# Performance work log

Measured on AMD Instinct MI355X. Metric: run time of the kernel, lower is better.

Reference implementation:

```python
import jax, jax.numpy as jnp
import numpy as np
import math

B, T, C = 1, 2048, 512
NH, NKV, HD, W = 8, 4, 64, 128  # heads, kv heads, head_dim, window_size
THETA = 10000.0
EPS = 1e-6


def _rms(x, w):
    # RMSNorm over last (head_dim) axis with learnable scale w
    return x * jax.lax.rsqrt(jnp.mean(x * x, axis=-1, keepdims=True) + EPS) * w


def _rope(x, cos, sin):
    # x: (B, H, T, HD); cos/sin: (T, HD//2). Half-split rotation.
    h = x.shape[-1] // 2
    x1, x2 = x[..., :h], x[..., h:]
    return jnp.concatenate([x1 * cos - x2 * sin, x2 * cos + x1 * sin], axis=-1)


def setup_inputs():
    key = jax.random.key(0)
    ks = jax.random.split(key, 5)
    x = jax.random.normal(ks[0], (B, T, C), jnp.float32)
    s = 1.0 / math.sqrt(C)
    W_q = jax.random.normal(ks[1], (C, NH * HD), jnp.float32) * s
    W_k = jax.random.normal(ks[2], (C, NKV * HD), jnp.float32) * s
    W_v = jax.random.normal(ks[3], (C, NKV * HD), jnp.float32) * s
    W_o = jax.random.normal(ks[4], (C, C), jnp.float32) * s
    q_norm_w = jnp.ones((HD,), jnp.float32)
    k_norm_w = jnp.ones((HD,), jnp.float32)
    pos = jnp.arange(T, dtype=jnp.float32)
    inv_freq = 1.0 / (THETA ** (jnp.arange(0, HD, 2, dtype=jnp.float32) / HD))
    ang = pos[:, None] * inv_freq[None, :]  # (T, HD//2)
    return {"x": x, "W_q": W_q, "W_k": W_k, "W_v": W_v, "W_o": W_o,
            "q_norm_w": q_norm_w, "k_norm_w": k_norm_w,
            "cos": jnp.cos(ang), "sin": jnp.sin(ang)}


def reference(x, W_q, W_k, W_v, W_o, q_norm_w, k_norm_w, cos, sin):
    q = (x @ W_q).reshape(B, T, NH, HD).transpose(0, 2, 1, 3)   # (B,NH,T,HD)
    k = (x @ W_k).reshape(B, T, NKV, HD).transpose(0, 2, 1, 3)  # (B,NKV,T,HD)
    v = (x @ W_v).reshape(B, T, NKV, HD).transpose(0, 2, 1, 3)
    q = _rope(q, cos, sin)
    k = _rope(k, cos, sin)
    q = _rms(q, q_norm_w)
    k = _rms(k, k_norm_w)
    g = NH // NKV  # GQA group size
    k = jnp.repeat(k, g, axis=1)  # (B,NH,T,HD)
    v = jnp.repeat(v, g, axis=1)
    # causal sliding-window: gather W-length windows ending at each position
    kp = jnp.pad(k, ((0, 0), (0, 0), (W - 1, 0), (0, 0)))
    vp = jnp.pad(v, ((0, 0), (0, 0), (W - 1, 0), (0, 0)))
    idx = jnp.arange(T)[:, None] + jnp.arange(W)[None, :]  # (T, W)
    kw = kp[:, :, idx, :]  # (B,NH,T,W,HD)
    vw = vp[:, :, idx, :]
    valid = jnp.arange(W)[None, :] >= (W - 1 - jnp.arange(T))[:, None]  # (T,W)
    attn = jnp.einsum('bhtd,bhtwd->bhtw', q, kw) / math.sqrt(HD)
    attn = jnp.where(valid[None, None], attn, -jnp.inf)
    attn = jax.nn.softmax(attn, axis=-1)
    out = jnp.einsum('bhtw,bhtwd->bhtd', attn, vw)  # (B,NH,T,HD)
    out = out.transpose(0, 2, 1, 3).reshape(B, T, C)
    return out @ W_o
```

## Files before the change

kernel.cpp:

```cpp
#include <hip/hip_runtime.h>
#include <hip/hip_bf16.h>
#include <math.h>

typedef float  f32x4  __attribute__((ext_vector_type(4)));
typedef short  s16x4  __attribute__((ext_vector_type(4)));
typedef short  s16x8  __attribute__((ext_vector_type(8)));
typedef unsigned short u16;

__device__ inline u16 f2b(float f) {
    __hip_bfloat16 h = __float2bfloat16(f);
    return *reinterpret_cast<u16*>(&h);
}
__device__ inline float b2f(u16 v) {
    return __uint_as_float(((unsigned)v) << 16);
}
__device__ inline void st_out(float* p, float v) { *p = v; }
__device__ inline void st_out(u16* p, float v)   { *p = f2b(v); }

__global__ __launch_bounds__(256) void prep(const float* __restrict__ x,
    const float* __restrict__ Wq, const float* __restrict__ Wk,
    const float* __restrict__ Wv, const float* __restrict__ Wo,
    u16* __restrict__ xb, u16* __restrict__ Wt, u16* __restrict__ Wot)
{
    const int tid = threadIdx.x, bid = blockIdx.x;
    if (bid >= 192) {
        int i = ((bid - 192) * 256 + tid) * 8;
        float4 v0 = *(const float4*)(x + i);
        float4 v1 = *(const float4*)(x + i + 4);
        ushort4 o0 = { f2b(v0.x), f2b(v0.y), f2b(v0.z), f2b(v0.w) };
        ushort4 o1 = { f2b(v1.x), f2b(v1.y), f2b(v1.z), f2b(v1.w) };
        *(ushort4*)(xb + i)     = o0;
        *(ushort4*)(xb + i + 4) = o1;
        return;
    }
    __shared__ u16 Tsh[64][72];
    const float* src; u16* dst; int N, base, kt, nt;
    if (bid < 64)       { src = Wq; dst = Wt;  N = 512; base = 0;   kt = bid >> 3;       nt = bid & 7; }
    else if (bid < 96)  { src = Wk; dst = Wt;  N = 256; base = 512; kt = (bid-64) >> 2;  nt = (bid-64) & 3; }
    else if (bid < 128) { src = Wv; dst = Wt;  N = 256; base = 768; kt = (bid-96) >> 2;  nt = (bid-96) & 3; }
    else                { src = Wo; dst = Wot; N = 512; base = 0;   kt = (bid-128) >> 3; nt = (bid-128) & 7; }
    const int k0 = kt * 64, n0 = nt * 64;
    const int r = tid >> 2, c0 = (tid & 3) * 16;
#pragma unroll
    for (int j = 0; j < 4; ++j) {
        float4 v = *(const float4*)(src + (size_t)(k0 + r) * N + n0 + c0 + j * 4);
        Tsh[c0 + j*4 + 0][r] = f2b(v.x);
        Tsh[c0 + j*4 + 1][r] = f2b(v.y);
        Tsh[c0 + j*4 + 2][r] = f2b(v.z);
        Tsh[c0 + j*4 + 3][r] = f2b(v.w);
    }
    __syncthreads();
    const int n = tid >> 2, kc = (tid & 3) * 16;
    u16* op = dst + (size_t)(base + n0 + n) * 512 + k0 + kc;
    *(s16x8*)(op)     = *(const s16x8*)&Tsh[n][kc];
    *(s16x8*)(op + 8) = *(const s16x8*)&Tsh[n][kc + 8];
}

template<typename OutT>
__global__ __launch_bounds__(256) void gemm_mfma(const u16* __restrict__ A,
    const u16* __restrict__ Bt, OutT* __restrict__ C, int ldc)
{
    __shared__ u16 Ash[64][72];
    __shared__ u16 Bsh[64][72];
    const int tid = threadIdx.x;
    const int m0b = blockIdx.y * 64, n0b = blockIdx.x * 64;
    const int lane = tid & 63, wv = tid >> 6;
    const int q = lane & 15, g = lane >> 4;
    const int wm = (wv & 1) * 32, wn = (wv >> 1) * 32;
    const int sr = tid >> 2, sc = (tid & 3) * 16;
    f32x4 acc[2][2] = {{{0,0,0,0},{0,0,0,0}},{{0,0,0,0},{0,0,0,0}}};
    for (int k0 = 0; k0 < 512; k0 += 64) {
        s16x8 a0 = *(const s16x8*)(A  + (size_t)(m0b + sr) * 512 + k0 + sc);
        s16x8 a1 = *(const s16x8*)(A  + (size_t)(m0b + sr) * 512 + k0 + sc + 8);
        s16x8 b0 = *(const s16x8*)(Bt + (size_t)(n0b + sr) * 512 + k0 + sc);
        s16x8 b1 = *(const s16x8*)(Bt + (size_t)(n0b + sr) * 512 + k0 + sc + 8);
        __syncthreads();
        *(s16x8*)&Ash[sr][sc]     = a0;
        *(s16x8*)&Ash[sr][sc + 8] = a1;
        *(s16x8*)&Bsh[sr][sc]     = b0;
        *(s16x8*)&Bsh[sr][sc + 8] = b1;
        __syncthreads();
#pragma unroll
        for (int kk = 0; kk < 64; kk += 32) {
            s16x8 af0 = *(const s16x8*)&Ash[wm + q][kk + g*8];
            s16x8 af1 = *(const s16x8*)&Ash[wm + 16 + q][kk + g*8];
            s16x8 bf0 = *(const s16x8*)&Bsh[wn + q][kk + g*8];
            s16x8 bf1 = *(const s16x8*)&Bsh[wn + 16 + q][kk + g*8];
            acc[0][0] = __builtin_amdgcn_mfma_f32_16x16x32_bf16(af0, bf0, acc[0][0], 0, 0, 0);
            acc[0][1] = __builtin_amdgcn_mfma_f32_16x16x32_bf16(af0, bf1, acc[0][1], 0, 0, 0);
            acc[1][0] = __builtin_amdgcn_mfma_f32_16x16x32_bf16(af1, bf0, acc[1][0], 0, 0, 0);
            acc[1][1] = __builtin_amdgcn_mfma_f32_16x16x32_bf16(af1, bf1, acc[1][1], 0, 0, 0);
        }
    }
#pragma unroll
    for (int mt = 0; mt < 2; ++mt)
#pragma unroll
        for (int nt = 0; nt < 2; ++nt)
#pragma unroll
            for (int r = 0; r < 4; ++r)
                st_out(&C[(size_t)(m0b + wm + mt*16 + g*4 + r) * ldc + n0b + wn + nt*16 + q],
                       acc[mt][nt][r]);
}

__global__ __launch_bounds__(256) void swa_mfma(const u16* __restrict__ qkvb,
    const float* __restrict__ cosT, const float* __restrict__ sinT,
    const float* __restrict__ qw, const float* __restrict__ kw,
    u16* __restrict__ attb)
{
    __shared__ u16 Ksh[192][72];
    __shared__ u16 Vt[64][202];
    const int tid = threadIdx.x;
    const int h = blockIdx.y, kvh = h >> 1;
    const int t0 = blockIdx.x * 64;
    for (int i = 0; i < 6; ++i) {
        int idx = i * 256 + tid;
        int j = idx >> 3, e = idx & 7, d0 = e * 8;
        int kt = t0 - 127 + j;
        if (kt < 0) {
            s16x8 z = {0,0,0,0,0,0,0,0};
            *(s16x8*)&Ksh[j][d0] = z;
        } else {
            s16x8 raw = *(const s16x8*)(qkvb + (size_t)kt * 1024 + 512 + kvh * 64 + d0);
            float kv[8], ov[8];
#pragma unroll
            for (int ii = 0; ii < 8; ++ii) kv[ii] = b2f((u16)raw[ii]);
#pragma unroll
            for (int ii = 0; ii < 8; ++ii) ov[ii] = __shfl_xor(kv[ii], 4);
            const float* cp = cosT + kt * 32 + (e & 3) * 8;
            const float* sp = sinT + kt * 32 + (e & 3) * 8;
            float4 c0 = *(const float4*)(cp),     c1 = *(const float4*)(cp + 4);
            float4 s0 = *(const float4*)(sp),     s1 = *(const float4*)(sp + 4);
            float cf[8] = {c0.x,c0.y,c0.z,c0.w,c1.x,c1.y,c1.z,c1.w};
            float sf[8] = {s0.x,s0.y,s0.z,s0.w,s1.x,s1.y,s1.z,s1.w};
            const bool lo = (e < 4);
            float r[8]; float ssl = 0.f;
#pragma unroll
            for (int ii = 0; ii < 8; ++ii) {
                r[ii] = lo ? (kv[ii]*cf[ii] - ov[ii]*sf[ii])
                           : (kv[ii]*cf[ii] + ov[ii]*sf[ii]);
                ssl += r[ii] * r[ii];
            }
            ssl += __shfl_xor(ssl, 1);
            ssl += __shfl_xor(ssl, 2);
            ssl += __shfl_xor(ssl, 4);
            float scale = rsqrtf(ssl * (1.0f / 64.0f) + 1e-6f);
            float4 w0 = *(const float4*)(kw + d0), w1 = *(const float4*)(kw + d0 + 4);
            float wf[8] = {w0.x,w0.y,w0.z,w0.w,w1.x,w1.y,w1.z,w1.w};
            s16x8 outv;
#pragma unroll
            for (int ii = 0; ii < 8; ++ii) outv[ii] = (short)f2b(r[ii] * scale * wf[ii]);
            *(s16x8*)&Ksh[j][d0] = outv;
        }
    }
    for (int cch = 0; cch < 6; ++cch) {
        int w  = cch * 32 + (tid & 31);
        int d0 = (tid >> 5) * 8;
        int kt = t0 - 127 + w;
        s16x8 val = {0,0,0,0,0,0,0,0};
        if (kt >= 0) val = *(const s16x8*)(qkvb + (size_t)kt * 1024 + 768 + kvh * 64 + d0);
#pragma unroll
        for (int jj = 0; jj < 8; ++jj) Vt[d0 + jj][w] = ((const u16*)&val)[jj];
    }
    const int wv = tid >> 6, lane = tid & 63;
    const int q = lane & 15, g = lane >> 4;
    const int tw = t0 + wv * 16;
    const int t = tw + q;
    s16x8 qf0, qf1;
    {
        const u16* qp = qkvb + (size_t)t * 1024 + h * 64;
        s16x8 q0r = *(const s16x8*)(qp + g * 8);
        s16x8 q1r = *(const s16x8*)(qp + 32 + g * 8);
        const float* cp = cosT + t * 32 + g * 8;
        const float* sp = sinT + t * 32 + g * 8;
        float4 c0 = *(const float4*)(cp), c1 = *(const float4*)(cp + 4);
        float4 s0 = *(const float4*)(sp), s1 = *(const float4*)(sp + 4);
        float cf[8] = {c0.x,c0.y,c0.z,c0.w,c1.x,c1.y,c1.z,c1.w};
        float sf[8] = {s0.x,s0.y,s0.z,s0.w,s1.x,s1.y,s1.z,s1.w};
        float rl[8], rh[8]; float ssl = 0.f;
#pragma unroll
        for (int ii = 0; ii < 8; ++ii) {
            float ql = b2f((u16)q0r[ii]), qh = b2f((u16)q1r[ii]);
            rl[ii] = ql * cf[ii] - qh * sf[ii];
            rh[ii] = qh * cf[ii] + ql * sf[ii];
            ssl += rl[ii]*rl[ii] + rh[ii]*rh[ii];
        }
        ssl += __shfl_xor(ssl, 16);
        ssl += __shfl_xor(ssl, 32);
        float scale = rsqrtf(ssl * (1.0f / 64.0f) + 1e-6f);
        float4 wl0 = *(const float4*)(qw + g * 8), wl1 = *(const float4*)(qw + g * 8 + 4);
        float4 wh0 = *(const float4*)(qw + 32 + g * 8), wh1 = *(const float4*)(qw + 32 + g * 8 + 4);
        float wlo[8] = {wl0.x,wl0.y,wl0.z,wl0.w,wl1.x,wl1.y,wl1.z,wl1.w};
        float whi[8] = {wh0.x,wh0.y,wh0.z,wh0.w,wh1.x,wh1.y,wh1.z,wh1.w};
#pragma unroll
        for (int ii = 0; ii < 8; ++ii) {
            qf0[ii] = (short)f2b(rl[ii] * scale * wlo[ii]);
            qf1[ii] = (short)f2b(rh[ii] * scale * whi[ii]);
        }
    }
    __syncthreads();
    float s[9][4];
    float mx = -INFINITY;
    for (int wt = 0; wt < 9; ++wt) {
        int ldsrow = wv * 16 + wt * 16 + q;
        s16x8 kf0 = *(const s16x8*)&Ksh[ldsrow][g * 8];
        s16x8 kf1 = *(const s16x8*)&Ksh[ldsrow][32 + g * 8];
        f32x4 accv = {0, 0, 0, 0};
        accv = __builtin_amdgcn_mfma_f32_16x16x32_bf16(kf0, qf0, accv, 0, 0, 0);
        accv = __builtin_amdgcn_mfma_f32_16x16x32_bf16(kf1, qf1, accv, 0, 0, 0);
#pragma unroll
        for (int r = 0; r < 4; ++r) {
            int woff = wt * 16 + g * 4 + r;
            int key  = tw - 127 + woff;
            bool ok = (woff >= q) && (woff <= q + 127) && (key >= 0);
            float sv = ok ? accv[r] * 0.125f : -INFINITY;
            s[wt][r] = sv;
            mx = fmaxf(mx, sv);
        }
    }
    mx = fmaxf(mx, __shfl_xor(mx, 16));
    mx = fmaxf(mx, __shfl_xor(mx, 32));
    float sum = 0.f;
    s16x4 pb[9];
    for (int wt = 0; wt < 9; ++wt) {
#pragma unroll
        for (int r = 0; r < 4; ++r) {
            float p = __expf(s[wt][r] - mx);
            sum += p;
            pb[wt][r] = (short)f2b(p);
        }
    }
    sum += __shfl_xor(sum, 16);
    sum += __shfl_xor(sum, 32);
    float inv = 1.0f / sum;
    f32x4 oacc[4];
#pragma unroll
    for (int dt = 0; dt < 4; ++dt) {
        f32x4 a = {0, 0, 0, 0};
        for (int wt = 0; wt < 9; ++wt) {
            int col = wv * 16 + wt * 16 + g * 4;
            s16x4 vf = *(const s16x4*)&Vt[dt * 16 + q][col];
            a = __builtin_amdgcn_mfma_f32_16x16x16bf16_1k(vf, pb[wt], a, 0, 0, 0);
        }
        oacc[dt] = a;
    }
    __syncthreads();
    float (*Osh)[16][68] = (float (*)[16][68])&Ksh[0][0];
#pragma unroll
    for (int dt = 0; dt < 4; ++dt)
#pragma unroll
        for (int r = 0; r < 4; ++r)
            Osh[wv][q][dt * 16 + g * 4 + r] = oacc[dt][r] * inv;
    __syncthreads();
    const int qq = lane >> 2, dd0 = (lane & 3) * 16;
    u16* op = attb + (size_t)(tw + qq) * 512 + h * 64 + dd0;
#pragma unroll
    for (int jj = 0; jj < 4; ++jj) {
        float4 vvv = *(const float4*)&Osh[wv][qq][dd0 + jj * 4];
        ushort4 ov = { f2b(vvv.x), f2b(vvv.y), f2b(vvv.z), f2b(vvv.w) };
        *(ushort4*)(op + jj * 4) = ov;
    }
}

extern "C" void kernel_launch(void* const* d_in, const int* in_sizes, int n_in,
                              void* d_out, int out_size, void* d_ws, size_t ws_size,
                              hipStream_t stream)
{
    const float* x    = (const float*)d_in[0];
    const float* Wq   = (const float*)d_in[1];
    const float* Wk   = (const float*)d_in[2];
    const float* Wv   = (const float*)d_in[3];
    const float* Wo   = (const float*)d_in[4];
    const float* qw   = (const float*)d_in[5];
    const float* kw   = (const float*)d_in[6];
    const float* cosT = (const float*)d_in[7];
    const float* sinT = (const float*)d_in[8];

    u16* ws   = (u16*)d_ws;
    u16* xb   = ws;
    u16* Wt   = xb   + (size_t)2048 * 512;
    u16* Wot  = Wt   + (size_t)1024 * 512;
    u16* qkvb = Wot  + (size_t)512 * 512;
    u16* attb = qkvb + (size_t)2048 * 1024;

    dim3 blk(256);
    hipLaunchKernelGGL(prep, dim3(704), blk, 0, stream, x, Wq, Wk, Wv, Wo, xb, Wt, Wot);
    hipLaunchKernelGGL((gemm_mfma<u16>), dim3(16, 32), blk, 0, stream, xb, Wt, qkvb, 1024);
    hipLaunchKernelGGL(swa_mfma, dim3(32, 8), blk, 0, stream,
                       qkvb, cosT, sinT, qw, kw, attb);
    hipLaunchKernelGGL((gemm_mfma<float>), dim3(8, 32), blk, 0, stream,
                       attb, Wot, (float*)d_out, 512);
}
```

Measured before the change: 35.47 us.

## Fuse x bf16 conversion into QKV GEMM and share K/V across GQA heads

The separate x-to-bf16 pass in the prep kernel is removed; the QKV GEMM now loads fp32 x directly and converts it while staging into LDS, which drops one write and one read of the activation buffer. The sliding-window attention kernel is regrouped so each block handles one KV head with both of its query heads over 32 query positions. K is RoPE-normalised once per block and V is transposed once per block, then reused by the two heads, and the grid grows to 64x4 blocks. In exchange the QKV GEMM re-converts x for every column tile, and the 127-row window halo is now a larger share of each smaller attention block.

```diff
diff --git a/kernel.cpp b/kernel.cpp
--- a/kernel.cpp
+++ b/kernel.cpp
@@ -14,25 +14,13 @@
 __device__ inline float b2f(u16 v) {
     return __uint_as_float(((unsigned)v) << 16);
 }
-__device__ inline void st_out(float* p, float v) { *p = v; }
-__device__ inline void st_out(u16* p, float v)   { *p = f2b(v); }
-
-__global__ __launch_bounds__(256) void prep(const float* __restrict__ x,
+
+__global__ __launch_bounds__(256) void prep(
     const float* __restrict__ Wq, const float* __restrict__ Wk,
     const float* __restrict__ Wv, const float* __restrict__ Wo,
-    u16* __restrict__ xb, u16* __restrict__ Wt, u16* __restrict__ Wot)
+    u16* __restrict__ Wt, u16* __restrict__ Wot)
 {
     const int tid = threadIdx.x, bid = blockIdx.x;
-    if (bid >= 192) {
-        int i = ((bid - 192) * 256 + tid) * 8;
-        float4 v0 = *(const float4*)(x + i);
-        float4 v1 = *(const float4*)(x + i + 4);
-        ushort4 o0 = { f2b(v0.x), f2b(v0.y), f2b(v0.z), f2b(v0.w) };
-        ushort4 o1 = { f2b(v1.x), f2b(v1.y), f2b(v1.z), f2b(v1.w) };
-        *(ushort4*)(xb + i)     = o0;
-        *(ushort4*)(xb + i + 4) = o1;
-        return;
-    }
     __shared__ u16 Tsh[64][72];
     const float* src; u16* dst; int N, base, kt, nt;
     if (bid < 64)       { src = Wq; dst = Wt;  N = 512; base = 0;   kt = bid >> 3;       nt = bid & 7; }
@@ -56,9 +44,8 @@
     *(s16x8*)(op + 8) = *(const s16x8*)&Tsh[n][kc + 8];
 }
 
-template<typename OutT>
-__global__ __launch_bounds__(256) void gemm_mfma(const u16* __restrict__ A,
-    const u16* __restrict__ Bt, OutT* __restrict__ C, int ldc)
+__global__ __launch_bounds__(256) void qkv_gemm(const float* __restrict__ x,
+    const u16* __restrict__ Bt, u16* __restrict__ C)
 {
     __shared__ u16 Ash[64][72];
     __shared__ u16 Bsh[64][72];
@@ -68,15 +55,28 @@
     const int q = lane & 15, g = lane >> 4;
     const int wm = (wv & 1) * 32, wn = (wv >> 1) * 32;
     const int sr = tid >> 2, sc = (tid & 3) * 16;
+    const float* xrow = x  + (size_t)(m0b + sr) * 512 + sc;
+    const u16*   Brow = Bt + (size_t)(n0b + sr) * 512 + sc;
     f32x4 acc[2][2] = {{{0,0,0,0},{0,0,0,0}},{{0,0,0,0},{0,0,0,0}}};
     for (int k0 = 0; k0 < 512; k0 += 64) {
-        s16x8 a0 = *(const s16x8*)(A  + (size_t)(m0b + sr) * 512 + k0 + sc);
-        s16x8 a1 = *(const s16x8*)(A  + (size_t)(m0b + sr) * 512 + k0 + sc + 8);
-        s16x8 b0 = *(const s16x8*)(Bt + (size_t)(n0b + sr) * 512 + k0 + sc);
-        s16x8 b1 = *(const s16x8*)(Bt + (size_t)(n0b + sr) * 512 + k0 + sc + 8);
+        float4 a0 = *(const float4*)(xrow + k0);
+        float4 a1 = *(const float4*)(xrow + k0 + 4);
+        float4 a2 = *(const float4*)(xrow + k0 + 8);
+        float4 a3 = *(const float4*)(xrow + k0 + 12);
+        s16x8 b0 = *(const s16x8*)(Brow + k0);
+        s16x8 b1 = *(const s16x8*)(Brow + k0 + 8);
+        s16x8 av0, av1;
+        av0[0] = (short)f2b(a0.x); av0[1] = (short)f2b(a0.y);
+        av0[2] = (short)f2b(a0.z); av0[3] = (short)f2b(a0.w);
+        av0[4] = (short)f2b(a1.x); av0[5] = (short)f2b(a1.y);
+        av0[6] = (short)f2b(a1.z); av0[7] = (short)f2b(a1.w);
+        av1[0] = (short)f2b(a2.x); av1[1] = (short)f2b(a2.y);
+        av1[2] = (short)f2b(a2.z); av1[3] = (short)f2b(a2.w);
+        av1[4] = (short)f2b(a3.x); av1[5] = (short)f2b(a3.y);
+        av1[6] = (short)f2b(a3.z); av1[7] = (short)f2b(a3.w);
         __syncthreads();
-        *(s16x8*)&Ash[sr][sc]     = a0;
-        *(s16x8*)&Ash[sr][sc + 8] = a1;
+        *(s16x8*)&Ash[sr][sc]     = av0;
+        *(s16x8*)&Ash[sr][sc + 8] = av1;
         *(s16x8*)&Bsh[sr][sc]     = b0;
         *(s16x8*)&Bsh[sr][sc + 8] = b1;
         __syncthreads();
@@ -98,8 +98,8 @@
         for (int nt = 0; nt < 2; ++nt)
 #pragma unroll
             for (int r = 0; r < 4; ++r)
-                st_out(&C[(size_t)(m0b + wm + mt*16 + g*4 + r) * ldc + n0b + wn + nt*16 + q],
-                       acc[mt][nt][r]);
+                C[(size_t)(m0b + wm + mt*16 + g*4 + r) * 1024 + n0b + wn + nt*16 + q] =
+                    f2b(acc[mt][nt][r]);
 }
 
 __global__ __launch_bounds__(256) void swa_mfma(const u16* __restrict__ qkvb,
@@ -107,16 +107,16 @@
     const float* __restrict__ qw, const float* __restrict__ kw,
     u16* __restrict__ attb)
 {
-    __shared__ u16 Ksh[192][72];
-    __shared__ u16 Vt[64][202];
+    __shared__ u16 Ksh[160][72];
+    __shared__ u16 Vt[64][162];
     const int tid = threadIdx.x;
-    const int h = blockIdx.y, kvh = h >> 1;
-    const int t0 = blockIdx.x * 64;
-    for (int i = 0; i < 6; ++i) {
+    const int kvh = blockIdx.y;
+    const int t0 = blockIdx.x * 32;
+    for (int i = 0; i < 5; ++i) {
         int idx = i * 256 + tid;
         int j = idx >> 3, e = idx & 7, d0 = e * 8;
         int kt = t0 - 127 + j;
-        if (kt < 0) {
+        if (kt < 0 || kt >= 2048) {
             s16x8 z = {0,0,0,0,0,0,0,0};
             *(s16x8*)&Ksh[j][d0] = z;
         } else {
@@ -128,8 +128,8 @@
             for (int ii = 0; ii < 8; ++ii) ov[ii] = __shfl_xor(kv[ii], 4);
             const float* cp = cosT + kt * 32 + (e & 3) * 8;
             const float* sp = sinT + kt * 32 + (e & 3) * 8;
-            float4 c0 = *(const float4*)(cp),     c1 = *(const float4*)(cp + 4);
-            float4 s0 = *(const float4*)(sp),     s1 = *(const float4*)(sp + 4);
+            float4 c0 = *(const float4*)(cp), c1 = *(const float4*)(cp + 4);
+            float4 s0 = *(const float4*)(sp), s1 = *(const float4*)(sp + 4);
             float cf[8] = {c0.x,c0.y,c0.z,c0.w,c1.x,c1.y,c1.z,c1.w};
             float sf[8] = {s0.x,s0.y,s0.z,s0.w,s1.x,s1.y,s1.z,s1.w};
             const bool lo = (e < 4);
@@ -152,18 +152,21 @@
             *(s16x8*)&Ksh[j][d0] = outv;
         }
     }
-    for (int cch = 0; cch < 6; ++cch) {
+    for (int cch = 0; cch < 5; ++cch) {
         int w  = cch * 32 + (tid & 31);
         int d0 = (tid >> 5) * 8;
         int kt = t0 - 127 + w;
         s16x8 val = {0,0,0,0,0,0,0,0};
-        if (kt >= 0) val = *(const s16x8*)(qkvb + (size_t)kt * 1024 + 768 + kvh * 64 + d0);
+        if (kt >= 0 && kt < 2048)
+            val = *(const s16x8*)(qkvb + (size_t)kt * 1024 + 768 + kvh * 64 + d0);
 #pragma unroll
         for (int jj = 0; jj < 8; ++jj) Vt[d0 + jj][w] = ((const u16*)&val)[jj];
     }
     const int wv = tid >> 6, lane = tid & 63;
     const int q = lane & 15, g = lane >> 4;
-    const int tw = t0 + wv * 16;
+    const int h  = 2 * kvh + (wv >> 1);
+    const int tw = t0 + (wv & 1) * 16;
+    const int jb = (wv & 1) * 16;
     const int t = tw + q;
     s16x8 qf0, qf1;
     {
@@ -201,7 +204,7 @@
     float s[9][4];
     float mx = -INFINITY;
     for (int wt = 0; wt < 9; ++wt) {
-        int ldsrow = wv * 16 + wt * 16 + q;
+        int ldsrow = jb + wt * 16 + q;
         s16x8 kf0 = *(const s16x8*)&Ksh[ldsrow][g * 8];
         s16x8 kf1 = *(const s16x8*)&Ksh[ldsrow][32 + g * 8];
         f32x4 accv = {0, 0, 0, 0};
@@ -237,7 +240,7 @@
     for (int dt = 0; dt < 4; ++dt) {
         f32x4 a = {0, 0, 0, 0};
         for (int wt = 0; wt < 9; ++wt) {
-            int col = wv * 16 + wt * 16 + g * 4;
+            int col = jb + wt * 16 + g * 4;
             s16x4 vf = *(const s16x4*)&Vt[dt * 16 + q][col];
             a = __builtin_amdgcn_mfma_f32_16x16x16bf16_1k(vf, pb[wt], a, 0, 0, 0);
         }
@@ -259,6 +262,50 @@
         ushort4 ov = { f2b(vvv.x), f2b(vvv.y), f2b(vvv.z), f2b(vvv.w) };
         *(ushort4*)(op + jj * 4) = ov;
     }
+}
+
+__global__ __launch_bounds__(256) void oproj(const u16* __restrict__ A,
+    const u16* __restrict__ Bt, float* __restrict__ C)
+{
+    __shared__ u16 Ash[64][72];
+    __shared__ u16 Bsh[64][72];
+    const int tid = threadIdx.x;
+    const int m0 = blockIdx.y * 64, n0 = blockIdx.x * 64;
+    const int lane = tid & 63, wv = tid >> 6;
+    const int q = lane & 15, g = lane >> 4;
+    const int wm = (wv & 1) * 32, wn = (wv >> 1) * 32;
+    const int sr = tid >> 2, sc = (tid & 3) * 16;
+    f32x4 acc[2][2] = {{{0,0,0,0},{0,0,0,0}},{{0,0,0,0},{0,0,0,0}}};
+    for (int k0 = 0; k0 < 512; k0 += 64) {
+        s16x8 a0 = *(const s16x8*)(A  + (size_t)(m0 + sr) * 512 + k0 + sc);
+        s16x8 a1 = *(const s16x8*)(A  + (size_t)(m0 + sr) * 512 + k0 + sc + 8);
+        s16x8 b0 = *(const s16x8*)(Bt + (size_t)(n0 + sr) * 512 + k0 + sc);
+        s16x8 b1 = *(const s16x8*)(Bt + (size_t)(n0 + sr) * 512 + k0 + sc + 8);
+        __syncthreads();
+        *(s16x8*)&Ash[sr][sc]     = a0;
+        *(s16x8*)&Ash[sr][sc + 8] = a1;
+        *(s16x8*)&Bsh[sr][sc]     = b0;
+        *(s16x8*)&Bsh[sr][sc + 8] = b1;
+        __syncthreads();
+#pragma unroll
+        for (int kk = 0; kk < 64; kk += 32) {
+            s16x8 af0 = *(const s16x8*)&Ash[wm + q][kk + g*8];
+            s16x8 af1 = *(const s16x8*)&Ash[wm + 16 + q][kk + g*8];
+            s16x8 bf0 = *(const s16x8*)&Bsh[wn + q][kk + g*8];
+            s16x8 bf1 = *(const s16x8*)&Bsh[wn + 16 + q][kk + g*8];
+            acc[0][0] = __builtin_amdgcn_mfma_f32_16x16x32_bf16(af0, bf0, acc[0][0], 0, 0, 0);
+            acc[0][1] = __builtin_amdgcn_mfma_f32_16x16x32_bf16(af0, bf1, acc[0][1], 0, 0, 0);
+            acc[1][0] = __builtin_amdgcn_mfma_f32_16x16x32_bf16(af1, bf0, acc[1][0], 0, 0, 0);
+            acc[1][1] = __builtin_amdgcn_mfma_f32_16x16x32_bf16(af1, bf1, acc[1][1], 0, 0, 0);
+        }
+    }
+#pragma unroll
+    for (int mt = 0; mt < 2; ++mt)
+#pragma unroll
+        for (int nt = 0; nt < 2; ++nt)
+#pragma unroll
+            for (int r = 0; r < 4; ++r)
+                C[(size_t)(m0 + wm + mt*16 + g*4 + r) * 512 + n0 + wn + nt*16 + q] = acc[mt][nt][r];
 }
 
 extern "C" void kernel_launch(void* const* d_in, const int* in_sizes, int n_in,
@@ -276,17 +323,15 @@
     const float* sinT = (const float*)d_in[8];
 
     u16* ws   = (u16*)d_ws;
-    u16* xb   = ws;
-    u16* Wt   = xb   + (size_t)2048 * 512;
+    u16* Wt   = ws;
     u16* Wot  = Wt   + (size_t)1024 * 512;
     u16* qkvb = Wot  + (size_t)512 * 512;
     u16* attb = qkvb + (size_t)2048 * 1024;
 
     dim3 blk(256);
-    hipLaunchKernelGGL(prep, dim3(704), blk, 0, stream, x, Wq, Wk, Wv, Wo, xb, Wt, Wot);
-    hipLaunchKernelGGL((gemm_mfma<u16>), dim3(16, 32), blk, 0, stream, xb, Wt, qkvb, 1024);
-    hipLaunchKernelGGL(swa_mfma, dim3(32, 8), blk, 0, stream,
+    hipLaunchKernelGGL(prep, dim3(192), blk, 0, stream, Wq, Wk, Wv, Wo, Wt, Wot);
+    hipLaunchKernelGGL(qkv_gemm, dim3(16, 32), blk, 0, stream, x, Wt, qkvb);
+    hipLaunchKernelGGL(swa_mfma, dim3(64, 4), blk, 0, stream,
                        qkvb, cosT, sinT, qw, kw, attb);
-    hipLaunchKernelGGL((gemm_mfma<float>), dim3(8, 32), blk, 0, stream,
-                       attb, Wot, (float*)d_out, 512);
-}
+    hipLaunchKernelGGL(oproj, dim3(8, 32), blk, 0, stream, attb, Wot, (float*)d_out);
+}
```

New measurement: 36.81 us. 1.04x slower.
